# Kernel tuning notes

Measured on AMD Instinct MI355X. Metric: run time of the kernel, lower is better.

The kernel has to match this reference:

```python
import jax, jax.numpy as jnp
import numpy as np

N = 100000      # nodes
E = 3200000     # edges (avg degree 32)
D_IN = 128      # input feature dim
H = 16          # hidden_size = GCN in/out channels
M = 16          # memory_size
SLOPE = 0.01    # F.leaky_relu default negative slope


def setup_inputs() -> dict:
    key = jax.random.key(0)
    ks = jax.random.split(key, 24)
    def p(i, shape):
        return jax.random.normal(ks[i], shape, dtype=jnp.float32) * 0.05
    return {
        "x": jax.random.normal(ks[0], (N, D_IN), dtype=jnp.float32),
        "edge_index": jax.random.randint(ks[1], (2, E), 0, N),
        # preprocess Linears (torch Linear: y = x @ W.T + b)
        "W1": p(2, (256, D_IN)), "b1": p(3, (256,)),
        "W2": p(4, (H, 256)),    "b2": p(5, (H,)),
        # EvolveGNN_O layer 1: memory buffer (zeros), GRU, weight_transform, GCN bias
        "mem1": jnp.zeros((M,), jnp.float32),
        "g1_Wih": p(6, (3 * M, M)), "g1_Whh": p(7, (3 * M, M)),
        "g1_bih": p(8, (3 * M,)),   "g1_bhh": p(9, (3 * M,)),
        "wt1_W": p(10, (H * H, M)), "wt1_b": p(11, (H * H,)),
        "gcn1_b": p(12, (H,)),
        # EvolveGNN_O layer 2
        "mem2": jnp.zeros((M,), jnp.float32),
        "g2_Wih": p(13, (3 * M, M)), "g2_Whh": p(14, (3 * M, M)),
        "g2_bih": p(15, (3 * M,)),   "g2_bhh": p(16, (3 * M,)),
        "wt2_W": p(17, (H * H, M)), "wt2_b": p(18, (H * H,)),
        "gcn2_b": p(19, (H,)),
        # postprocessing Linear(hidden, 2)
        "Wout": p(20, (2, H)), "bout": p(21, (2,)),
    }


def _leaky(x):
    return jnp.where(x >= 0, x, SLOPE * x)


def _gru_step(x, Wih, Whh, bih, bhh):
    # PyTorch nn.GRU single step, h0 = 0 (default when h not provided)
    h = jnp.zeros_like(x)
    gi = Wih @ x + bih
    gh = Whh @ h + bhh
    ir, iz, inn = jnp.split(gi, 3)
    hr, hz, hn = jnp.split(gh, 3)
    r = jax.nn.sigmoid(ir + hr)
    z = jax.nn.sigmoid(iz + hz)
    n = jnp.tanh(inn + r * hn)
    return (1.0 - z) * n + z * h


def _gcn(h, row, col, W, bias):
    # PyG GCNConv: linear transform, symmetric gcn_norm (self-loops already
    # appended to row/col), gather from row, scatter-add to col, add bias.
    n = h.shape[0]
    xl = h @ W.T                                          # [N, H]
    ones = jnp.ones(row.shape[0], h.dtype)
    deg = jax.ops.segment_sum(ones, col, num_segments=n)  # in-degree incl. self-loop
    dis = jnp.where(deg > 0, jax.lax.rsqrt(deg), 0.0)
    norm = dis[row] * dis[col]                            # [E + N]
    out = jax.ops.segment_sum(xl[row] * norm[:, None], col, num_segments=n)
    return out + bias


def _evolve_gcn(h, row, col, mem, Wih, Whh, bih, bhh, wtW, wtb, gcn_b):
    new_mem = _gru_step(mem, Wih, Whh, bih, bhh)          # GRU-updated memory
    Wnew = (wtW @ new_mem + wtb).reshape(H, H)            # regenerated lin.weight [out, in]
    return _gcn(h, row, col, Wnew, gcn_b)


def reference(x, edge_index, W1, b1, W2, b2,
              mem1, g1_Wih, g1_Whh, g1_bih, g1_bhh, wt1_W, wt1_b, gcn1_b,
              mem2, g2_Wih, g2_Whh, g2_bih, g2_bhh, wt2_W, wt2_b, gcn2_b,
              Wout, bout):
    n = x.shape[0]
    loops = jnp.arange(n, dtype=edge_index.dtype)
    row = jnp.concatenate([edge_index[0], loops])         # sources (+ self-loops)
    col = jnp.concatenate([edge_index[1], loops])         # targets (+ self-loops)

    h = _leaky(x @ W1.T + b1)                             # [N, 256]
    h = _leaky(h @ W2.T + b2)                             # [N, 16]
    h = _leaky(_evolve_gcn(h, row, col, mem1, g1_Wih, g1_Whh, g1_bih, g1_bhh, wt1_W, wt1_b, gcn1_b))
    h = _leaky(_evolve_gcn(h, row, col, mem2, g2_Wih, g2_Whh, g2_bih, g2_bhh, wt2_W, wt2_b, gcn2_b))
    h = h @ Wout.T + bout                                 # [N, 2]
    return jnp.sum(h, axis=-1)                            # [N]
```

## Files before the change

### kernel.cpp

```cpp
#include <hip/hip_runtime.h>
#include <math.h>

#define SLOPE 0.01f
#define BKS   256
#define BSH2  8
#define NBKMAX 512
#define BCAP  10240

typedef short  bf16x8 __attribute__((ext_vector_type(8)));
typedef float  f32x4  __attribute__((ext_vector_type(4)));

__device__ __forceinline__ float lrelu(float v) { return v >= 0.f ? v : SLOPE * v; }

__device__ __forceinline__ unsigned short f2bf(float v) {
    unsigned u = __float_as_uint(v);
    return (unsigned short)((u + 0x7FFFu + ((u >> 16) & 1u)) >> 16);
}
__device__ __forceinline__ float bf2f(unsigned short b) {
    return __uint_as_float(((unsigned)b) << 16);
}

__global__ void prep_k(const float* __restrict__ m1, const float* __restrict__ Wih1,
                       const float* __restrict__ bih1, const float* __restrict__ bhh1,
                       const float* __restrict__ m2, const float* __restrict__ Wih2,
                       const float* __restrict__ bih2, const float* __restrict__ bhh2,
                       const float* __restrict__ wtW1, const float* __restrict__ wtb1,
                       const float* __restrict__ wtW2, const float* __restrict__ wtb2,
                       const float* __restrict__ Wout, const float* __restrict__ bout,
                       const float* __restrict__ W2,
                       float* __restrict__ Wn1, float* __restrict__ Wn2,
                       float* __restrict__ wsum, float* __restrict__ bsum,
                       unsigned short* __restrict__ W2bh, unsigned short* __restrict__ W2bl,
                       int* __restrict__ bfill, int NBK) {
    __shared__ float nm[32];
    int t = threadIdx.x;
    if (t < 32) {
        int L = t >> 4, j = t & 15;
        const float* m   = L ? m2   : m1;
        const float* Wih = L ? Wih2 : Wih1;
        const float* bih = L ? bih2 : bih1;
        const float* bhh = L ? bhh2 : bhh1;
        float gr = bih[j], gz = bih[16 + j], gn = bih[32 + j];
        for (int k = 0; k < 16; ++k) {
            float mk = m[k];
            gr += Wih[j * 16 + k] * mk;
            gz += Wih[(16 + j) * 16 + k] * mk;
            gn += Wih[(32 + j) * 16 + k] * mk;
        }
        float r = 1.f / (1.f + expf(-(gr + bhh[j])));
        float z = 1.f / (1.f + expf(-(gz + bhh[16 + j])));
        float n = tanhf(gn + r * bhh[32 + j]);
        nm[t] = (1.f - z) * n;
    }
    __syncthreads();
    float s1 = wtb1[t], s2 = wtb2[t];
    for (int k = 0; k < 16; ++k) {
        s1 += wtW1[t * 16 + k] * nm[k];
        s2 += wtW2[t * 16 + k] * nm[16 + k];
    }
    Wn1[t] = s1;
    Wn2[t] = s2;
    for (int i = t; i < 4096; i += 256) {
        float v = W2[i];
        unsigned short h = f2bf(v);
        W2bh[i] = h;
        W2bl[i] = f2bf(v - bf2f(h));
    }
    if (t < 16) wsum[t] = Wout[t] + Wout[16 + t];
    if (t == 0) bsum[0] = bout[0] + bout[1];
    for (int i = t; i < NBK; i += 256) bfill[i] = i * BCAP;
}

__global__ void wsplit_k(const float* __restrict__ W1,
                         unsigned short* __restrict__ W1h,
                         unsigned short* __restrict__ W1l) {
    int i = blockIdx.x * 256 + threadIdx.x;
    float v = W1[i];
    unsigned short h = f2bf(v);
    W1h[i] = h;
    W1l[i] = f2bf(v - bf2f(h));
}

__global__ void bscat_k(const int* __restrict__ row, const int* __restrict__ col,
                        int* __restrict__ bfill, int2* __restrict__ stage,
                        int E, int NBK) {
    __shared__ int lcnt[NBKMAX];
    __shared__ int lbase[NBKMAX];
    int t = threadIdx.x;
    for (int i = t; i < NBK; i += 256) lcnt[i] = 0;
    __syncthreads();
    int base = blockIdx.x * 4096;
    int r[16], d[16], sl[16];
#pragma unroll
    for (int i = 0; i < 16; ++i) {
        int e = base + i * 256 + t;
        if (e < E) {
            r[i]  = row[e];
            d[i]  = col[e];
            sl[i] = atomicAdd(&lcnt[d[i] >> BSH2], 1);
        } else d[i] = -1;
    }
    __syncthreads();
    for (int i = t; i < NBK; i += 256)
        lbase[i] = lcnt[i] ? atomicAdd(bfill + i, lcnt[i]) : 0;
    __syncthreads();
#pragma unroll
    for (int i = 0; i < 16; ++i) {
        if (d[i] >= 0)
            stage[lbase[d[i] >> BSH2] + sl[i]] = make_int2(r[i], d[i]);
    }
}

__global__ __launch_bounds__(512) void cscan_k(const int* __restrict__ bfill,
                                               int* __restrict__ bbase2,
                                               int* __restrict__ off,
                                               int NBK, int N, int E) {
    __shared__ int s[512];
    int t = threadIdx.x;
    int v = (t < NBK) ? (bfill[t] - t * BCAP) : 0;
    s[t] = v;
    __syncthreads();
    for (int d = 1; d < 512; d <<= 1) {
        int u = (t >= d) ? s[t - d] : 0;
        __syncthreads();
        s[t] += u;
        __syncthreads();
    }
    if (t < NBK) bbase2[t] = s[t] - v;
    if (t == 0) { bbase2[NBK] = E; off[N] = E; }
}

__global__ void bproc_k(const int2* __restrict__ stage, const int* __restrict__ bbase2,
                        int* __restrict__ off, float* __restrict__ dis,
                        int* __restrict__ srcs, int N) {
    __shared__ int lh[BKS];
    __shared__ int ssc[BKS];
    const int b  = blockIdx.x;
    const int t  = threadIdx.x;
    const int sb = b * BCAP;
    const int e0 = bbase2[b];
    const int cnt = bbase2[b + 1] - e0;
    lh[t] = 0;
    __syncthreads();
    for (int i = t; i < cnt; i += 256) {
        int2 v = stage[sb + i];
        atomicAdd(&lh[v.y & (BKS - 1)], 1);
    }
    __syncthreads();
    int c = lh[t];
    ssc[t] = c;
    __syncthreads();
    for (int d = 1; d < 256; d <<= 1) {
        int u = (t >= d) ? ssc[t - d] : 0;
        __syncthreads();
        ssc[t] += u;
        __syncthreads();
    }
    int ex = ssc[t] - c;
    {
        int node = b * BKS + t;
        if (node < N) {
            off[node] = e0 + ex;
            dis[node] = rsqrtf((float)(c + 1));
        }
    }
    __syncthreads();
    lh[t] = ex;
    __syncthreads();
    for (int i = t; i < cnt; i += 256) {
        int2 w = stage[sb + i];
        int pos = e0 + atomicAdd(&lh[w.y & (BKS - 1)], 1);
        srcs[pos] = w.x;
    }
}

__global__ __launch_bounds__(512, 4) void mlp_k(
        const float* __restrict__ x,
        const unsigned short* __restrict__ W1h,
        const unsigned short* __restrict__ W1l,
        const float* __restrict__ b1,
        const unsigned short* __restrict__ W2bh,
        const unsigned short* __restrict__ W2bl,
        const float* __restrict__ b2,
        const float* __restrict__ Wn1,
        const float* __restrict__ dis,
        unsigned short* __restrict__ xl, int N) {
    __shared__ float sbuf[19456];
    unsigned short* xh  = (unsigned short*)sbuf;
    unsigned short* xlo = xh + 8704;
    unsigned short* h1h = (unsigned short*)sbuf;
    unsigned short* h1l = h1h + 16896;
    float*          h2p = sbuf + 16896;

    const int t      = threadIdx.x;
    const int nl     = t & 63;
    const int q      = __builtin_amdgcn_readfirstlane(t >> 6);
    const int lane15 = t & 15;
    const int quad   = (t & 63) >> 4;
    const int node   = blockIdx.x * 64 + nl;
    const bool valid = node < N;

    float4 xv[4];
    if (valid) {
        const float4* xr = (const float4*)(x + (size_t)node * 128) + q * 4;
#pragma unroll
        for (int kk = 0; kk < 4; ++kk) xv[kk] = xr[kk];
    }

    bf16x8 w1hf[2][4], w1lf[2][4];
#pragma unroll
    for (int nt = 0; nt < 2; ++nt)
#pragma unroll
        for (int ks = 0; ks < 4; ++ks) {
            size_t wo = (size_t)(q * 32 + nt * 16 + lane15) * 128 + ks * 32 + quad * 8;
            w1hf[nt][ks] = *(const bf16x8*)(W1h + wo);
            w1lf[nt][ks] = *(const bf16x8*)(W1l + wo);
        }

    {
        unsigned* xh32 = (unsigned*)xh;
        unsigned* xl32 = (unsigned*)xlo;
        int base = nl * 68 + q * 8;
        if (valid) {
#pragma unroll
            for (int kk = 0; kk < 4; ++kk) {
                float4 v = xv[kk];
                unsigned short hx = f2bf(v.x), hy = f2bf(v.y);
                unsigned short hz = f2bf(v.z), hw = f2bf(v.w);
                unsigned short lx = f2bf(v.x - bf2f(hx)), ly = f2bf(v.y - bf2f(hy));
                unsigned short lz = f2bf(v.z - bf2f(hz)), lw = f2bf(v.w - bf2f(hw));
                *(uint2*)(xh32 + base + kk * 2) =
                    make_uint2((unsigned)hx | ((unsigned)hy << 16),
                               (unsigned)hz | ((unsigned)hw << 16));
                *(uint2*)(xl32 + base + kk * 2) =
                    make_uint2((unsigned)lx | ((unsigned)ly << 16),
                               (unsigned)lz | ((unsigned)lw << 16));
            }
        } else {
#pragma unroll
            for (int kk = 0; kk < 4; ++kk) {
                *(uint2*)(xh32 + base + kk * 2) = make_uint2(0u, 0u);
                *(uint2*)(xl32 + base + kk * 2) = make_uint2(0u, 0u);
            }
        }
    }
    __syncthreads();

    f32x4 acc[4][2];
#pragma unroll
    for (int mt = 0; mt < 4; ++mt)
#pragma unroll
        for (int nt = 0; nt < 2; ++nt)
            acc[mt][nt] = (f32x4){0.f, 0.f, 0.f, 0.f};

#pragma unroll
    for (int ks = 0; ks < 4; ++ks) {
        const int koff = ks * 32 + quad * 8;
#pragma unroll
        for (int mt = 0; mt < 4; ++mt) {
            bf16x8 ah = *(const bf16x8*)(xh  + (16 * mt + lane15) * 136 + koff);
            bf16x8 al = *(const bf16x8*)(xlo + (16 * mt + lane15) * 136 + koff);
#pragma unroll
            for (int nt = 0; nt < 2; ++nt) {
                acc[mt][nt] = __builtin_amdgcn_mfma_f32_16x16x32_bf16(ah, w1hf[nt][ks], acc[mt][nt], 0, 0, 0);
                acc[mt][nt] = __builtin_amdgcn_mfma_f32_16x16x32_bf16(ah, w1lf[nt][ks], acc[mt][nt], 0, 0, 0);
                acc[mt][nt] = __builtin_amdgcn_mfma_f32_16x16x32_bf16(al, w1hf[nt][ks], acc[mt][nt], 0, 0, 0);
            }
        }
    }
    __syncthreads();

    const int kh  = q >> 2;
    const int mt2 = q & 3;
    bf16x8 w2hf[4], w2lf[4];
#pragma unroll
    for (int ks2 = 0; ks2 < 4; ++ks2) {
        int wo = lane15 * 256 + (kh * 4 + ks2) * 32 + quad * 8;
        w2hf[ks2] = *(const bf16x8*)(W2bh + wo);
        w2lf[ks2] = *(const bf16x8*)(W2bl + wo);
    }

#pragma unroll
    for (int nt = 0; nt < 2; ++nt) {
        int hu = q * 32 + nt * 16 + lane15;
        float bb = b1[hu];
#pragma unroll
        for (int mt = 0; mt < 4; ++mt) {
            int row0 = 16 * mt + quad * 4;
#pragma unroll
            for (int r = 0; r < 4; ++r) {
                float v = lrelu(acc[mt][nt][r] + bb);
                unsigned short h = f2bf(v);
                h1h[(row0 + r) * 264 + hu] = h;
                h1l[(row0 + r) * 264 + hu] = f2bf(v - bf2f(h));
            }
        }
    }
    __syncthreads();

    f32x4 a2 = (f32x4){0.f, 0.f, 0.f, 0.f};
#pragma unroll
    for (int ks2 = 0; ks2 < 4; ++ks2) {
        const int koff = (kh * 4 + ks2) * 32 + quad * 8;
        bf16x8 ah = *(const bf16x8*)(h1h + (16 * mt2 + lane15) * 264 + koff);
        bf16x8 al = *(const bf16x8*)(h1l + (16 * mt2 + lane15) * 264 + koff);
        a2 = __builtin_amdgcn_mfma_f32_16x16x32_bf16(ah, w2hf[ks2], a2, 0, 0, 0);
        a2 = __builtin_amdgcn_mfma_f32_16x16x32_bf16(ah, w2lf[ks2], a2, 0, 0, 0);
        a2 = __builtin_amdgcn_mfma_f32_16x16x32_bf16(al, w2hf[ks2], a2, 0, 0, 0);
    }
    {
        float* dst = h2p + kh * 1280 + (16 * mt2 + quad * 4) * 20 + lane15;
        dst[0] = a2[0]; dst[20] = a2[1]; dst[40] = a2[2]; dst[60] = a2[3];
    }
    __syncthreads();

    {
        const f32x4* pa = (const f32x4*)(h2p + nl * 20);
        const f32x4* pb = (const f32x4*)(h2p + 1280 + nl * 20);
        f32x4 s[4];
#pragma unroll
        for (int i = 0; i < 4; ++i) s[i] = pa[i] + pb[i];
        float o0 = 0.f, o1 = 0.f;
        const float* wr0 = Wn1 + (2 * q) * 16;
        const float* wr1 = Wn1 + (2 * q + 1) * 16;
#pragma unroll
        for (int j = 0; j < 16; ++j) {
            float h = lrelu(s[j >> 2][j & 3] + b2[j]);
            o0 = fmaf(wr0[j], h, o0);
            o1 = fmaf(wr1[j], h, o1);
        }
        if (valid) {
            float d = dis[node];
            unsigned pk = (unsigned)f2bf(d * o0) | ((unsigned)f2bf(d * o1) << 16);
            *(unsigned*)(xl + (size_t)node * 16 + 2 * q) = pk;
        }
    }
}

__global__ void gather1_k(const int* __restrict__ off, const int* __restrict__ srcs,
                          const float* __restrict__ dis,
                          const unsigned short* __restrict__ xin,
                          const float* __restrict__ bias, const float* __restrict__ Wn2,
                          unsigned short* __restrict__ xout, int N) {
    __shared__ float w[256];
    {
        int j = threadIdx.x >> 4, c = threadIdx.x & 15;
        w[threadIdx.x] = Wn2[c * 16 + j];
    }
    __syncthreads();
    int t = blockIdx.x * 256 + threadIdx.x;
    int n = t >> 6;
    if (n >= N) return;
    int lane = t & 63, sub = lane >> 4, c = lane & 15;
    float acc = (sub == 0) ? bf2f(xin[(size_t)n * 16 + c]) : 0.f;
    int e  = off[n] + sub;
    int e1 = off[n + 1];
    for (; e + 12 < e1; e += 16) {
        int s0 = srcs[e], s1 = srcs[e + 4], s2 = srcs[e + 8], s3 = srcs[e + 12];
        float v0 = bf2f(xin[(size_t)s0 * 16 + c]);
        float v1 = bf2f(xin[(size_t)s1 * 16 + c]);
        float v2 = bf2f(xin[(size_t)s2 * 16 + c]);
        float v3 = bf2f(xin[(size_t)s3 * 16 + c]);
        acc += (v0 + v1) + (v2 + v3);
    }
    for (; e < e1; e += 4)
        acc += bf2f(xin[(size_t)srcs[e] * 16 + c]);
    acc += __shfl_xor(acc, 16);
    acc += __shfl_xor(acc, 32);
    float d = dis[n];
    float h = lrelu(fmaf(d, acc, bias[c]));
    float o = 0.f;
#pragma unroll
    for (int j = 0; j < 16; ++j) o = fmaf(w[j * 16 + c], __shfl(h, j, 16), o);
    if (sub == 0) xout[(size_t)n * 16 + c] = f2bf(d * o);
}

__global__ void gather2_k(const int* __restrict__ off, const int* __restrict__ srcs,
                          const float* __restrict__ dis,
                          const unsigned short* __restrict__ xin,
                          const float* __restrict__ bias, const float* __restrict__ wsum,
                          const float* __restrict__ bsum, float* __restrict__ out, int N) {
    int t = blockIdx.x * 256 + threadIdx.x;
    int n = t >> 6;
    if (n >= N) return;
    int lane = t & 63, sub = lane >> 4, c = lane & 15;
    float acc = (sub == 0) ? bf2f(xin[(size_t)n * 16 + c]) : 0.f;
    int e  = off[n] + sub;
    int e1 = off[n + 1];
    for (; e + 12 < e1; e += 16) {
        int s0 = srcs[e], s1 = srcs[e + 4], s2 = srcs[e + 8], s3 = srcs[e + 12];
        float v0 = bf2f(xin[(size_t)s0 * 16 + c]);
        float v1 = bf2f(xin[(size_t)s1 * 16 + c]);
        float v2 = bf2f(xin[(size_t)s2 * 16 + c]);
        float v3 = bf2f(xin[(size_t)s3 * 16 + c]);
        acc += (v0 + v1) + (v2 + v3);
    }
    for (; e < e1; e += 4)
        acc += bf2f(xin[(size_t)srcs[e] * 16 + c]);
    acc += __shfl_xor(acc, 16);
    acc += __shfl_xor(acc, 32);
    float v = wsum[c] * lrelu(fmaf(dis[n], acc, bias[c]));
#pragma unroll
    for (int m = 1; m < 16; m <<= 1) v += __shfl_xor(v, m);
    if (lane == 0) out[n] = v + bsum[0];
}

extern "C" void kernel_launch(void* const* d_in, const int* in_sizes, int n_in,
                              void* d_out, int out_size, void* d_ws, size_t ws_size,
                              hipStream_t stream) {
    const float* x      = (const float*)d_in[0];
    const int*   edge   = (const int*)d_in[1];
    const float* W1     = (const float*)d_in[2];
    const float* b1     = (const float*)d_in[3];
    const float* W2     = (const float*)d_in[4];
    const float* b2     = (const float*)d_in[5];
    const float* mem1   = (const float*)d_in[6];
    const float* g1_Wih = (const float*)d_in[7];
    const float* g1_bih = (const float*)d_in[9];
    const float* g1_bhh = (const float*)d_in[10];
    const float* wt1_W  = (const float*)d_in[11];
    const float* wt1_b  = (const float*)d_in[12];
    const float* gcn1_b = (const float*)d_in[13];
    const float* mem2   = (const float*)d_in[14];
    const float* g2_Wih = (const float*)d_in[15];
    const float* g2_bih = (const float*)d_in[17];
    const float* g2_bhh = (const float*)d_in[18];
    const float* wt2_W  = (const float*)d_in[19];
    const float* wt2_b  = (const float*)d_in[20];
    const float* gcn2_b = (const float*)d_in[21];
    const float* Wout   = (const float*)d_in[22];
    const float* bout   = (const float*)d_in[23];
    float* out = (float*)d_out;

    const int N = in_sizes[0] / 128;
    const int E = in_sizes[1] / 2;
    const int* row = edge;
    const int* col = edge + E;

    const int NBK = (N + BKS - 1) >> BSH2;
    const int gM  = (N + 63) / 64;
    const int gG  = (N * 64 + 255) / 256;
    const int gB  = (E + 4095) / 4096;

    float* ws    = (float*)d_ws;
    float* bufA  = ws;
    float* bufB  = bufA + (size_t)N * 16;
    float* dis   = bufB + (size_t)N * 16;
    float* sm    = dis + N;
    float* Wn1   = sm;
    float* Wn2   = sm + 256;
    float* wsum  = sm + 512;
    float* bsum  = sm + 528;
    unsigned short* W2bh = (unsigned short*)(sm + 544);
    unsigned short* W2bl = (unsigned short*)(sm + 2592);
    unsigned short* W1h = (unsigned short*)(sm + 4640);
    unsigned short* W1l = (unsigned short*)(sm + 21024);
    int*   bfill = (int*)(sm + 37408);
    int*   bbase2= bfill + NBKMAX;
    int*   off   = bbase2 + NBKMAX + 1;
    int*   srcs  = off + N + 1;
    size_t stoff = (size_t)(srcs + E - (int*)d_ws);
    stoff = (stoff + 3) & ~(size_t)3;
    int2*  stage = (int2*)((int*)d_ws + stoff);

    prep_k<<<1, 256, 0, stream>>>(mem1, g1_Wih, g1_bih, g1_bhh,
                                  mem2, g2_Wih, g2_bih, g2_bhh,
                                  wt1_W, wt1_b, wt2_W, wt2_b,
                                  Wout, bout, W2, Wn1, Wn2, wsum, bsum,
                                  W2bh, W2bl, bfill, NBK);
    wsplit_k<<<128, 256, 0, stream>>>(W1, W1h, W1l);
    bscat_k<<<gB, 256, 0, stream>>>(row, col, bfill, stage, E, NBK);
    cscan_k<<<1, 512, 0, stream>>>(bfill, bbase2, off, NBK, N, E);
    bproc_k<<<NBK, 256, 0, stream>>>(stage, bbase2, off, dis, srcs, N);
    mlp_k<<<gM, 512, 0, stream>>>(x, W1h, W1l, b1, W2bh, W2bl, b2, Wn1, dis,
                                  (unsigned short*)bufA, N);
    gather1_k<<<gG, 256, 0, stream>>>(off, srcs, dis, (unsigned short*)bufA,
                                      gcn1_b, Wn2, (unsigned short*)bufB, N);
    gather2_k<<<gG, 256, 0, stream>>>(off, srcs, dis, (unsigned short*)bufB,
                                      gcn2_b, wsum, bsum, out, N);
}
```

Measured before the change: 375.5 us.

## Shrink MLP kernel LDS and registers, drop low-part of hidden activations

Removes the low-order bf16 split of the first hidden layer, so the second GEMM uses two MFMAs per step instead of three and LDS shrinks enough to raise the launch-bounds occupancy target from 4 to 6. W1 fragments are now loaded from global/cache inside the MFMA loop instead of being held in registers. The x tile is loaded cooperatively with coalesced float4 reads. This lowers register and LDS pressure at the cost of precision in the hidden activations and repeated weight loads.

```diff
diff --git a/kernel.cpp b/kernel.cpp
--- a/kernel.cpp
+++ b/kernel.cpp
@@ -174,7 +174,7 @@
     }
 }
 
-__global__ __launch_bounds__(512, 4) void mlp_k(
+__global__ __launch_bounds__(512, 6) void mlp_k(
         const float* __restrict__ x,
         const unsigned short* __restrict__ W1h,
         const unsigned short* __restrict__ W1l,
@@ -185,12 +185,11 @@
         const float* __restrict__ Wn1,
         const float* __restrict__ dis,
         unsigned short* __restrict__ xl, int N) {
-    __shared__ float sbuf[19456];
+    __shared__ float sbuf[11008];
     unsigned short* xh  = (unsigned short*)sbuf;
     unsigned short* xlo = xh + 8704;
     unsigned short* h1h = (unsigned short*)sbuf;
-    unsigned short* h1l = h1h + 16896;
-    float*          h2p = sbuf + 16896;
+    float*          h2p = sbuf + 8448;
 
     const int t      = threadIdx.x;
     const int nl     = t & 63;
@@ -200,48 +199,29 @@
     const int node   = blockIdx.x * 64 + nl;
     const bool valid = node < N;
 
-    float4 xv[4];
-    if (valid) {
-        const float4* xr = (const float4*)(x + (size_t)node * 128) + q * 4;
-#pragma unroll
-        for (int kk = 0; kk < 4; ++kk) xv[kk] = xr[kk];
-    }
-
-    bf16x8 w1hf[2][4], w1lf[2][4];
-#pragma unroll
-    for (int nt = 0; nt < 2; ++nt)
-#pragma unroll
-        for (int ks = 0; ks < 4; ++ks) {
-            size_t wo = (size_t)(q * 32 + nt * 16 + lane15) * 128 + ks * 32 + quad * 8;
-            w1hf[nt][ks] = *(const bf16x8*)(W1h + wo);
-            w1lf[nt][ks] = *(const bf16x8*)(W1l + wo);
-        }
-
     {
+        const float4* x4 = (const float4*)x;
+        const size_t tb = (size_t)blockIdx.x * 2048;
         unsigned* xh32 = (unsigned*)xh;
         unsigned* xl32 = (unsigned*)xlo;
-        int base = nl * 68 + q * 8;
-        if (valid) {
-#pragma unroll
-            for (int kk = 0; kk < 4; ++kk) {
-                float4 v = xv[kk];
-                unsigned short hx = f2bf(v.x), hy = f2bf(v.y);
-                unsigned short hz = f2bf(v.z), hw = f2bf(v.w);
-                unsigned short lx = f2bf(v.x - bf2f(hx)), ly = f2bf(v.y - bf2f(hy));
-                unsigned short lz = f2bf(v.z - bf2f(hz)), lw = f2bf(v.w - bf2f(hw));
-                *(uint2*)(xh32 + base + kk * 2) =
-                    make_uint2((unsigned)hx | ((unsigned)hy << 16),
-                               (unsigned)hz | ((unsigned)hw << 16));
-                *(uint2*)(xl32 + base + kk * 2) =
-                    make_uint2((unsigned)lx | ((unsigned)ly << 16),
-                               (unsigned)lz | ((unsigned)lw << 16));
-            }
-        } else {
-#pragma unroll
-            for (int kk = 0; kk < 4; ++kk) {
-                *(uint2*)(xh32 + base + kk * 2) = make_uint2(0u, 0u);
-                *(uint2*)(xl32 + base + kk * 2) = make_uint2(0u, 0u);
-            }
+#pragma unroll
+        for (int kk = 0; kk < 4; ++kk) {
+            int idx  = kk * 512 + t;
+            int row  = idx >> 5;
+            int col4 = idx & 31;
+            float4 v = make_float4(0.f, 0.f, 0.f, 0.f);
+            if (blockIdx.x * 64 + row < N) v = x4[tb + idx];
+            unsigned short hx = f2bf(v.x), hy = f2bf(v.y);
+            unsigned short hz = f2bf(v.z), hw = f2bf(v.w);
+            unsigned short lx = f2bf(v.x - bf2f(hx)), ly = f2bf(v.y - bf2f(hy));
+            unsigned short lz = f2bf(v.z - bf2f(hz)), lw = f2bf(v.w - bf2f(hw));
+            int base = row * 68 + col4 * 2;
+            *(uint2*)(xh32 + base) =
+                make_uint2((unsigned)hx | ((unsigned)hy << 16),
+                           (unsigned)hz | ((unsigned)hw << 16));
+            *(uint2*)(xl32 + base) =
+                make_uint2((unsigned)lx | ((unsigned)ly << 16),
+                           (unsigned)lz | ((unsigned)lw << 16));
         }
     }
     __syncthreads();
@@ -262,9 +242,12 @@
             bf16x8 al = *(const bf16x8*)(xlo + (16 * mt + lane15) * 136 + koff);
 #pragma unroll
             for (int nt = 0; nt < 2; ++nt) {
-                acc[mt][nt] = __builtin_amdgcn_mfma_f32_16x16x32_bf16(ah, w1hf[nt][ks], acc[mt][nt], 0, 0, 0);
-                acc[mt][nt] = __builtin_amdgcn_mfma_f32_16x16x32_bf16(ah, w1lf[nt][ks], acc[mt][nt], 0, 0, 0);
-                acc[mt][nt] = __builtin_amdgcn_mfma_f32_16x16x32_bf16(al, w1hf[nt][ks], acc[mt][nt], 0, 0, 0);
+                size_t wo = (size_t)(q * 32 + nt * 16 + lane15) * 128 + koff;
+                bf16x8 bh = *(const bf16x8*)(W1h + wo);
+                bf16x8 bl = *(const bf16x8*)(W1l + wo);
+                acc[mt][nt] = __builtin_amdgcn_mfma_f32_16x16x32_bf16(ah, bh, acc[mt][nt], 0, 0, 0);
+                acc[mt][nt] = __builtin_amdgcn_mfma_f32_16x16x32_bf16(ah, bl, acc[mt][nt], 0, 0, 0);
+                acc[mt][nt] = __builtin_amdgcn_mfma_f32_16x16x32_bf16(al, bh, acc[mt][nt], 0, 0, 0);
             }
         }
     }
@@ -290,9 +273,7 @@
 #pragma unroll
             for (int r = 0; r < 4; ++r) {
                 float v = lrelu(acc[mt][nt][r] + bb);
-                unsigned short h = f2bf(v);
-                h1h[(row0 + r) * 264 + hu] = h;
-                h1l[(row0 + r) * 264 + hu] = f2bf(v - bf2f(h));
+                h1h[(row0 + r) * 264 + hu] = f2bf(v);
             }
         }
     }
@@ -303,10 +284,8 @@
     for (int ks2 = 0; ks2 < 4; ++ks2) {
         const int koff = (kh * 4 + ks2) * 32 + quad * 8;
         bf16x8 ah = *(const bf16x8*)(h1h + (16 * mt2 + lane15) * 264 + koff);
-        bf16x8 al = *(const bf16x8*)(h1l + (16 * mt2 + lane15) * 264 + koff);
         a2 = __builtin_amdgcn_mfma_f32_16x16x32_bf16(ah, w2hf[ks2], a2, 0, 0, 0);
         a2 = __builtin_amdgcn_mfma_f32_16x16x32_bf16(ah, w2lf[ks2], a2, 0, 0, 0);
-        a2 = __builtin_amdgcn_mfma_f32_16x16x32_bf16(al, w2hf[ks2], a2, 0, 0, 0);
     }
     {
         float* dst = h2p + kh * 1280 + (16 * mt2 + quad * 4) * 20 + lane15;
```

Measured after the change: 369.8 us. About the same (-1.5%).
